# Kernel tuning notes

Measured on AMD Instinct MI355X. Metric: run time of the kernel, lower is better.

## Reference

```python
import jax, jax.numpy as jnp
import numpy as np

N = 100000      # nodes
E = 1600000     # edges (avg degree 16)
F_IN = 512      # nfeat
C = 64          # nclass


def setup_inputs() -> dict:
    key = jax.random.key(0)
    k1, k2, k3 = jax.random.split(key, 3)
    x = jax.random.normal(k1, (N, F_IN), dtype=jnp.float32)
    edge_index = jax.random.randint(k2, (2, E), 0, N, dtype=jnp.int32)
    # GCNConv weight (glorot-ish) and bias
    W = jax.random.normal(k3, (F_IN, C), dtype=jnp.float32) * (1.0 / np.sqrt(F_IN))
    b = jnp.zeros((C,), dtype=jnp.float32)
    return {"x": x, "W": W, "b": b, "edge_index": edge_index}


def reference(x, W, b, edge_index):
    # Standard GCNConv (sheaf_laplacian=None): project, add self-loops,
    # symmetric normalization D^{-1/2}(A+I)D^{-1/2}, aggregate, bias.
    h = x @ W  # [N, C] project first (C < F_IN), as torch_geometric does
    self_loops = jnp.arange(N, dtype=edge_index.dtype)
    src = jnp.concatenate([edge_index[0], self_loops])
    dst = jnp.concatenate([edge_index[1], self_loops])
    deg = jax.ops.segment_sum(jnp.ones_like(dst, dtype=h.dtype), dst, num_segments=N)
    dinv = jnp.where(deg > 0, jax.lax.rsqrt(deg), 0.0)  # deg^{-1/2}
    norm = dinv[src] * dinv[dst]  # [E+N]
    msgs = h[src] * norm[:, None]  # gather + scale, [E+N, C]
    out = jax.ops.segment_sum(msgs, dst, num_segments=N) + b  # [N, C]
    return jax.nn.log_softmax(out, axis=1)
```

## Files before the change

kernel.cpp:

```cpp
#include <hip/hip_runtime.h>
#include <hip/hip_bf16.h>

#define F_IN 512
#define NCLS 64
#define SCAN_BLK 512

typedef __attribute__((ext_vector_type(8))) short short8;
typedef __attribute__((ext_vector_type(4))) float f32x4;

static __device__ __forceinline__ short bf16_of(float f) {
    __hip_bfloat16 h = __float2bfloat16(f);
    short s;
    __builtin_memcpy(&s, &h, 2);
    return s;
}
static __device__ __forceinline__ float b2f(short s) {
    unsigned u = ((unsigned)(unsigned short)s) << 16;
    float f;
    __builtin_memcpy(&f, &u, 4);
    return f;
}

__global__ __launch_bounds__(256) void prelude(const float* __restrict__ W,
                                               short* __restrict__ Wb,
                                               int* __restrict__ cnt, int n) {
    const int bid = blockIdx.x;
    if (bid < 16) {
        int t = bid * 256 + threadIdx.x;
        int c = t >> 10;
        int kk = (t >> 6) & 15;
        int l = t & 63;
        short8 v;
#pragma unroll
        for (int j = 0; j < 8; ++j) {
            v[j] = bf16_of(W[(size_t)(kk * 32 + (l >> 4) * 8 + j) * NCLS + c * 16 + (l & 15)]);
        }
        reinterpret_cast<short8*>(Wb)[t] = v;
    } else {
        int i = (bid - 16) * 256 + threadIdx.x;
        if (i < n) cnt[i] = 0;
    }
}

__global__ __launch_bounds__(256) void megaA(const float* __restrict__ x,
                                             const short* __restrict__ Wb,
                                             short* __restrict__ g, int n,
                                             const int* __restrict__ dst,
                                             int* __restrict__ cnt,
                                             unsigned short* __restrict__ rank, int e,
                                             int gemmBlocks, int degBlocks) {
    const int bid = blockIdx.x;
    const int m2 = 2 * (gemmBlocks < degBlocks ? gemmBlocks : degBlocks);
    int role, idx;
    if (bid < m2) { role = bid & 1; idx = bid >> 1; }
    else if (gemmBlocks > degBlocks) { role = 0; idx = bid - degBlocks; }
    else { role = 1; idx = bid - gemmBlocks; }

    if (role == 1) {
        int base = (idx * 256 + threadIdx.x) * 4;
        if (base + 4 <= e) {
            int4 d4 = *reinterpret_cast<const int4*>(dst + base);
            ushort4 r;
            r.x = (unsigned short)atomicAdd(&cnt[d4.x], 1);
            r.y = (unsigned short)atomicAdd(&cnt[d4.y], 1);
            r.z = (unsigned short)atomicAdd(&cnt[d4.z], 1);
            r.w = (unsigned short)atomicAdd(&cnt[d4.w], 1);
            *reinterpret_cast<ushort4*>(rank + base) = r;
        } else {
            for (int i = base; i < e; ++i)
                rank[i] = (unsigned short)atomicAdd(&cnt[dst[i]], 1);
        }
        return;
    }

    const int wave = threadIdx.x >> 6;
    const int lane = threadIdx.x & 63;
    const int rowTile = idx * 64 + wave * 16;

    int arow = rowTile + (lane & 15);
    if (arow > n - 1) arow = n - 1;
    const float* xr = x + (size_t)arow * F_IN + ((lane >> 4) * 8);

    const short8* wb8 = reinterpret_cast<const short8*>(Wb);

    f32x4 acc0 = {0.f, 0.f, 0.f, 0.f};
    f32x4 acc1 = {0.f, 0.f, 0.f, 0.f};
    f32x4 acc2 = {0.f, 0.f, 0.f, 0.f};
    f32x4 acc3 = {0.f, 0.f, 0.f, 0.f};

#pragma unroll 4
    for (int kk = 0; kk < 16; ++kk) {
        float4 f0 = *reinterpret_cast<const float4*>(xr + kk * 32);
        float4 f1 = *reinterpret_cast<const float4*>(xr + kk * 32 + 4);
        short8 a;
        a[0] = bf16_of(f0.x); a[1] = bf16_of(f0.y);
        a[2] = bf16_of(f0.z); a[3] = bf16_of(f0.w);
        a[4] = bf16_of(f1.x); a[5] = bf16_of(f1.y);
        a[6] = bf16_of(f1.z); a[7] = bf16_of(f1.w);
        short8 b0 = wb8[(0 * 16 + kk) * 64 + lane];
        short8 b1 = wb8[(1 * 16 + kk) * 64 + lane];
        short8 b2 = wb8[(2 * 16 + kk) * 64 + lane];
        short8 b3 = wb8[(3 * 16 + kk) * 64 + lane];
        acc0 = __builtin_amdgcn_mfma_f32_16x16x32_bf16(a, b0, acc0, 0, 0, 0);
        acc1 = __builtin_amdgcn_mfma_f32_16x16x32_bf16(a, b1, acc1, 0, 0, 0);
        acc2 = __builtin_amdgcn_mfma_f32_16x16x32_bf16(a, b2, acc2, 0, 0, 0);
        acc3 = __builtin_amdgcn_mfma_f32_16x16x32_bf16(a, b3, acc3, 0, 0, 0);
    }

    const int col = lane & 15;
    const int rbase = rowTile + (lane >> 4) * 4;
#pragma unroll
    for (int j = 0; j < 4; ++j) {
        int r = rbase + j;
        if (r < n) {
            short* go = g + (size_t)r * NCLS + col;
            go[0]  = bf16_of(acc0[j]);
            go[16] = bf16_of(acc1[j]);
            go[32] = bf16_of(acc2[j]);
            go[48] = bf16_of(acc3[j]);
        }
    }
}

__global__ __launch_bounds__(SCAN_BLK) void scan1(const int* __restrict__ cnt,
                                                  int* __restrict__ off,
                                                  int* __restrict__ partials,
                                                  float* __restrict__ dinv, int n) {
    __shared__ int s[SCAN_BLK];
    int tid = threadIdx.x;
    int i = blockIdx.x * SCAN_BLK + tid;
    int v = (i < n) ? cnt[i] : 0;
    if (i < n) dinv[i] = rsqrtf(1.0f + (float)v);
    s[tid] = v;
    __syncthreads();
#pragma unroll
    for (int d = 1; d < SCAN_BLK; d <<= 1) {
        int t = (tid >= d) ? s[tid - d] : 0;
        __syncthreads();
        s[tid] += t;
        __syncthreads();
    }
    if (i < n) off[i] = s[tid] - v;
    if (i == n - 1) off[n] = s[tid];
    if (tid == SCAN_BLK - 1) partials[blockIdx.x] = s[tid];
}

__global__ __launch_bounds__(256) void scan2(int* __restrict__ partials, int p) {
    __shared__ int s[256];
    int tid = threadIdx.x;
    int v = (tid < p) ? partials[tid] : 0;
    s[tid] = v;
    __syncthreads();
#pragma unroll
    for (int d = 1; d < 256; d <<= 1) {
        int t = (tid >= d) ? s[tid - d] : 0;
        __syncthreads();
        s[tid] += t;
        __syncthreads();
    }
    if (tid < p) partials[tid] = s[tid] - v;
}

__global__ __launch_bounds__(256) void fill_csr(const int* __restrict__ src,
                                                const int* __restrict__ dst,
                                                const int* __restrict__ off,
                                                const int* __restrict__ parts,
                                                const unsigned short* __restrict__ rank,
                                                int* __restrict__ eidx, int e) {
    int base = (blockIdx.x * 256 + threadIdx.x) * 4;
    if (base + 4 <= e) {
        int4 s4 = *reinterpret_cast<const int4*>(src + base);
        int4 d4 = *reinterpret_cast<const int4*>(dst + base);
        ushort4 r4 = *reinterpret_cast<const ushort4*>(rank + base);
        eidx[off[d4.x] + parts[d4.x >> 9] + r4.x] = s4.x;
        eidx[off[d4.y] + parts[d4.y >> 9] + r4.y] = s4.y;
        eidx[off[d4.z] + parts[d4.z >> 9] + r4.z] = s4.z;
        eidx[off[d4.w] + parts[d4.w >> 9] + r4.w] = s4.w;
    } else {
        for (int i = base; i < e; ++i)
            eidx[off[dst[i]] + parts[dst[i] >> 9] + rank[i]] = src[i];
    }
}

__global__ __launch_bounds__(256) void aggregate(const short* __restrict__ g,
                                                 const float* __restrict__ dinv,
                                                 const float* __restrict__ b,
                                                 const int* __restrict__ off,
                                                 const int* __restrict__ parts,
                                                 const int* __restrict__ eidx,
                                                 float* __restrict__ out, int n) {
    const int wave = threadIdx.x >> 6;
    const int lane = threadIdx.x & 63;
    const int grp = lane >> 3;
    const int li = lane & 7;
    const int node = (blockIdx.x * 4 + wave) * 8 + grp;
    if (node >= n) return;

    const int s0 = off[node] + parts[node >> 9];
    const int np1 = node + 1;
    const int s1 = off[np1] + parts[(np1 == n ? n - 1 : np1) >> 9];

    const short8* g8 = reinterpret_cast<const short8*>(g);
    const float dn = dinv[node];

    float acc[8];
    {
        short8 v = g8[(size_t)node * 8 + li];
#pragma unroll
        for (int c = 0; c < 8; ++c) acc[c] = b2f(v[c]) * dn;
    }

    int t = s0;
    for (; t + 4 <= s1; t += 4) {
        int sa = eidx[t];
        int sb = eidx[t + 1];
        int sc = eidx[t + 2];
        int sd = eidx[t + 3];
        float da = dinv[sa], db = dinv[sb], dc = dinv[sc], dd = dinv[sd];
        short8 va = g8[(size_t)sa * 8 + li];
        short8 vb = g8[(size_t)sb * 8 + li];
        short8 vc = g8[(size_t)sc * 8 + li];
        short8 vd = g8[(size_t)sd * 8 + li];
#pragma unroll
        for (int c = 0; c < 8; ++c)
            acc[c] += (b2f(va[c]) * da + b2f(vb[c]) * db) + (b2f(vc[c]) * dc + b2f(vd[c]) * dd);
    }
    for (; t < s1; ++t) {
        int sa = eidx[t];
        float da = dinv[sa];
        short8 va = g8[(size_t)sa * 8 + li];
#pragma unroll
        for (int c = 0; c < 8; ++c) acc[c] += b2f(va[c]) * da;
    }

    const float4 b0 = reinterpret_cast<const float4*>(b)[li * 2];
    const float4 b1 = reinterpret_cast<const float4*>(b)[li * 2 + 1];
    float v[8];
    v[0] = acc[0] * dn + b0.x; v[1] = acc[1] * dn + b0.y;
    v[2] = acc[2] * dn + b0.z; v[3] = acc[3] * dn + b0.w;
    v[4] = acc[4] * dn + b1.x; v[5] = acc[5] * dn + b1.y;
    v[6] = acc[6] * dn + b1.z; v[7] = acc[7] * dn + b1.w;

    float m = v[0];
#pragma unroll
    for (int c = 1; c < 8; ++c) m = fmaxf(m, v[c]);
#pragma unroll
    for (int o = 1; o < 8; o <<= 1) m = fmaxf(m, __shfl_xor(m, o));

    float ex = 0.f;
#pragma unroll
    for (int c = 0; c < 8; ++c) ex += __expf(v[c] - m);
#pragma unroll
    for (int o = 1; o < 8; o <<= 1) ex += __shfl_xor(ex, o);
    const float lg = m + __logf(ex);

    float4 r0, r1;
    r0.x = v[0] - lg; r0.y = v[1] - lg; r0.z = v[2] - lg; r0.w = v[3] - lg;
    r1.x = v[4] - lg; r1.y = v[5] - lg; r1.z = v[6] - lg; r1.w = v[7] - lg;
    float4* o4 = reinterpret_cast<float4*>(out + (size_t)node * NCLS);
    o4[li * 2] = r0;
    o4[li * 2 + 1] = r1;
}

extern "C" void kernel_launch(void* const* d_in, const int* in_sizes, int n_in,
                              void* d_out, int out_size, void* d_ws, size_t ws_size,
                              hipStream_t stream) {
    const float* x = (const float*)d_in[0];
    const float* W = (const float*)d_in[1];
    const float* b = (const float*)d_in[2];
    const int* edge_index = (const int*)d_in[3];

    const int N = in_sizes[0] / F_IN;
    const int E = in_sizes[3] / 2;
    const int* src = edge_index;
    const int* dst = edge_index + E;

    float* out = (float*)d_out;

    char* ws = (char*)d_ws;
    short* g     = (short*)ws;  ws += (size_t)N * NCLS * 2;
    short* Wb    = (short*)ws;  ws += 4096 * 16;
    float* dinv  = (float*)ws;  ws += (size_t)N * 4;
    int*   cnt   = (int*)ws;    ws += (size_t)N * 4;
    int*   off   = (int*)ws;    ws += (size_t)(N + 4) * 4;
    int*   parts = (int*)ws;    ws += 1024 * 4;
    unsigned short* rank = (unsigned short*)ws;  ws += (size_t)((E + 7) & ~7) * 2;
    int*   eidx  = (int*)ws;

    const int nScanBlocks = (N + SCAN_BLK - 1) / SCAN_BLK;
    const int gemmBlocks = (N + 63) / 64;
    const int degBlocks = (E + 1023) / 1024;

    prelude<<<16 + (N + 255) / 256, 256, 0, stream>>>(W, Wb, cnt, N);

    megaA<<<gemmBlocks + degBlocks, 256, 0, stream>>>(x, Wb, g, N, dst, cnt, rank, E,
                                                      gemmBlocks, degBlocks);

    scan1<<<nScanBlocks, SCAN_BLK, 0, stream>>>(cnt, off, parts, dinv, N);
    scan2<<<1, 256, 0, stream>>>(parts, nScanBlocks);

    fill_csr<<<degBlocks, 256, 0, stream>>>(src, dst, off, parts, rank, eidx, E);

    aggregate<<<(N + 31) / 32, 256, 0, stream>>>(g, dinv, b, off, parts, eidx, out, N);
}
```

Baseline: 186.5 us.

## Fold source-degree scaling into GEMM epilogue and split degree count from GEMM

The megaA kernel, which interleaved GEMM blocks with degree-counting blocks, is split in two. The GEMM now runs after the degree scan, so each projected row can be pre-scaled by dinv[src] before it is stored in bf16. This removes the per-edge dinv gather from aggregation, whose inner loop is also widened to 8 edges for more memory-level parallelism. The GEMM tile grows to 32 rows per wave to reuse W loads. The cost is losing the overlap between the GEMM and the atomic degree counting, since they are now serialized.

```diff
diff --git a/kernel.cpp b/kernel.cpp
--- a/kernel.cpp
+++ b/kernel.cpp
@@ -42,83 +42,21 @@
     }
 }
 
-__global__ __launch_bounds__(256) void megaA(const float* __restrict__ x,
-                                             const short* __restrict__ Wb,
-                                             short* __restrict__ g, int n,
-                                             const int* __restrict__ dst,
-                                             int* __restrict__ cnt,
-                                             unsigned short* __restrict__ rank, int e,
-                                             int gemmBlocks, int degBlocks) {
-    const int bid = blockIdx.x;
-    const int m2 = 2 * (gemmBlocks < degBlocks ? gemmBlocks : degBlocks);
-    int role, idx;
-    if (bid < m2) { role = bid & 1; idx = bid >> 1; }
-    else if (gemmBlocks > degBlocks) { role = 0; idx = bid - degBlocks; }
-    else { role = 1; idx = bid - gemmBlocks; }
-
-    if (role == 1) {
-        int base = (idx * 256 + threadIdx.x) * 4;
-        if (base + 4 <= e) {
-            int4 d4 = *reinterpret_cast<const int4*>(dst + base);
-            ushort4 r;
-            r.x = (unsigned short)atomicAdd(&cnt[d4.x], 1);
-            r.y = (unsigned short)atomicAdd(&cnt[d4.y], 1);
-            r.z = (unsigned short)atomicAdd(&cnt[d4.z], 1);
-            r.w = (unsigned short)atomicAdd(&cnt[d4.w], 1);
-            *reinterpret_cast<ushort4*>(rank + base) = r;
-        } else {
-            for (int i = base; i < e; ++i)
-                rank[i] = (unsigned short)atomicAdd(&cnt[dst[i]], 1);
-        }
-        return;
-    }
-
-    const int wave = threadIdx.x >> 6;
-    const int lane = threadIdx.x & 63;
-    const int rowTile = idx * 64 + wave * 16;
-
-    int arow = rowTile + (lane & 15);
-    if (arow > n - 1) arow = n - 1;
-    const float* xr = x + (size_t)arow * F_IN + ((lane >> 4) * 8);
-
-    const short8* wb8 = reinterpret_cast<const short8*>(Wb);
-
-    f32x4 acc0 = {0.f, 0.f, 0.f, 0.f};
-    f32x4 acc1 = {0.f, 0.f, 0.f, 0.f};
-    f32x4 acc2 = {0.f, 0.f, 0.f, 0.f};
-    f32x4 acc3 = {0.f, 0.f, 0.f, 0.f};
-
-#pragma unroll 4
-    for (int kk = 0; kk < 16; ++kk) {
-        float4 f0 = *reinterpret_cast<const float4*>(xr + kk * 32);
-        float4 f1 = *reinterpret_cast<const float4*>(xr + kk * 32 + 4);
-        short8 a;
-        a[0] = bf16_of(f0.x); a[1] = bf16_of(f0.y);
-        a[2] = bf16_of(f0.z); a[3] = bf16_of(f0.w);
-        a[4] = bf16_of(f1.x); a[5] = bf16_of(f1.y);
-        a[6] = bf16_of(f1.z); a[7] = bf16_of(f1.w);
-        short8 b0 = wb8[(0 * 16 + kk) * 64 + lane];
-        short8 b1 = wb8[(1 * 16 + kk) * 64 + lane];
-        short8 b2 = wb8[(2 * 16 + kk) * 64 + lane];
-        short8 b3 = wb8[(3 * 16 + kk) * 64 + lane];
-        acc0 = __builtin_amdgcn_mfma_f32_16x16x32_bf16(a, b0, acc0, 0, 0, 0);
-        acc1 = __builtin_amdgcn_mfma_f32_16x16x32_bf16(a, b1, acc1, 0, 0, 0);
-        acc2 = __builtin_amdgcn_mfma_f32_16x16x32_bf16(a, b2, acc2, 0, 0, 0);
-        acc3 = __builtin_amdgcn_mfma_f32_16x16x32_bf16(a, b3, acc3, 0, 0, 0);
-    }
-
-    const int col = lane & 15;
-    const int rbase = rowTile + (lane >> 4) * 4;
-#pragma unroll
-    for (int j = 0; j < 4; ++j) {
-        int r = rbase + j;
-        if (r < n) {
-            short* go = g + (size_t)r * NCLS + col;
-            go[0]  = bf16_of(acc0[j]);
-            go[16] = bf16_of(acc1[j]);
-            go[32] = bf16_of(acc2[j]);
-            go[48] = bf16_of(acc3[j]);
-        }
+__global__ __launch_bounds__(256) void deg_count(const int* __restrict__ dst,
+                                                 int* __restrict__ cnt,
+                                                 unsigned short* __restrict__ rank, int e) {
+    int base = (blockIdx.x * 256 + threadIdx.x) * 4;
+    if (base + 4 <= e) {
+        int4 d4 = *reinterpret_cast<const int4*>(dst + base);
+        ushort4 r;
+        r.x = (unsigned short)atomicAdd(&cnt[d4.x], 1);
+        r.y = (unsigned short)atomicAdd(&cnt[d4.y], 1);
+        r.z = (unsigned short)atomicAdd(&cnt[d4.z], 1);
+        r.w = (unsigned short)atomicAdd(&cnt[d4.w], 1);
+        *reinterpret_cast<ushort4*>(rank + base) = r;
+    } else {
+        for (int i = base; i < e; ++i)
+            rank[i] = (unsigned short)atomicAdd(&cnt[dst[i]], 1);
     }
 }
 
@@ -182,6 +120,77 @@
     }
 }
 
+__global__ __launch_bounds__(256) void gemm_mfma(const float* __restrict__ x,
+                                                 const short* __restrict__ Wb,
+                                                 const float* __restrict__ dinv,
+                                                 short* __restrict__ g, int n) {
+    const int wave = threadIdx.x >> 6;
+    const int lane = threadIdx.x & 63;
+    const int rowTile = blockIdx.x * 128 + wave * 32;
+
+    int r0 = rowTile + (lane & 15);
+    int r1 = r0 + 16;
+    if (r0 > n - 1) r0 = n - 1;
+    if (r1 > n - 1) r1 = n - 1;
+    const float* xr0 = x + (size_t)r0 * F_IN + ((lane >> 4) * 8);
+    const float* xr1 = x + (size_t)r1 * F_IN + ((lane >> 4) * 8);
+
+    const short8* wb8 = reinterpret_cast<const short8*>(Wb);
+
+    f32x4 acc[2][4];
+#pragma unroll
+    for (int h = 0; h < 2; ++h)
+#pragma unroll
+        for (int c = 0; c < 4; ++c) acc[h][c] = {0.f, 0.f, 0.f, 0.f};
+
+#pragma unroll 4
+    for (int kk = 0; kk < 16; ++kk) {
+        float4 p0 = *reinterpret_cast<const float4*>(xr0 + kk * 32);
+        float4 p1 = *reinterpret_cast<const float4*>(xr0 + kk * 32 + 4);
+        float4 q0 = *reinterpret_cast<const float4*>(xr1 + kk * 32);
+        float4 q1 = *reinterpret_cast<const float4*>(xr1 + kk * 32 + 4);
+        short8 a0, a1;
+        a0[0] = bf16_of(p0.x); a0[1] = bf16_of(p0.y);
+        a0[2] = bf16_of(p0.z); a0[3] = bf16_of(p0.w);
+        a0[4] = bf16_of(p1.x); a0[5] = bf16_of(p1.y);
+        a0[6] = bf16_of(p1.z); a0[7] = bf16_of(p1.w);
+        a1[0] = bf16_of(q0.x); a1[1] = bf16_of(q0.y);
+        a1[2] = bf16_of(q0.z); a1[3] = bf16_of(q0.w);
+        a1[4] = bf16_of(q1.x); a1[5] = bf16_of(q1.y);
+        a1[6] = bf16_of(q1.z); a1[7] = bf16_of(q1.w);
+        short8 b0 = wb8[(0 * 16 + kk) * 64 + lane];
+        short8 b1 = wb8[(1 * 16 + kk) * 64 + lane];
+        short8 b2 = wb8[(2 * 16 + kk) * 64 + lane];
+        short8 b3 = wb8[(3 * 16 + kk) * 64 + lane];
+        acc[0][0] = __builtin_amdgcn_mfma_f32_16x16x32_bf16(a0, b0, acc[0][0], 0, 0, 0);
+        acc[0][1] = __builtin_amdgcn_mfma_f32_16x16x32_bf16(a0, b1, acc[0][1], 0, 0, 0);
+        acc[0][2] = __builtin_amdgcn_mfma_f32_16x16x32_bf16(a0, b2, acc[0][2], 0, 0, 0);
+        acc[0][3] = __builtin_amdgcn_mfma_f32_16x16x32_bf16(a0, b3, acc[0][3], 0, 0, 0);
+        acc[1][0] = __builtin_amdgcn_mfma_f32_16x16x32_bf16(a1, b0, acc[1][0], 0, 0, 0);
+        acc[1][1] = __builtin_amdgcn_mfma_f32_16x16x32_bf16(a1, b1, acc[1][1], 0, 0, 0);
+        acc[1][2] = __builtin_amdgcn_mfma_f32_16x16x32_bf16(a1, b2, acc[1][2], 0, 0, 0);
+        acc[1][3] = __builtin_amdgcn_mfma_f32_16x16x32_bf16(a1, b3, acc[1][3], 0, 0, 0);
+    }
+
+    const int col = lane & 15;
+#pragma unroll
+    for (int h = 0; h < 2; ++h) {
+        const int rbase = rowTile + h * 16 + (lane >> 4) * 4;
+#pragma unroll
+        for (int j = 0; j < 4; ++j) {
+            int r = rbase + j;
+            if (r < n) {
+                float dv = dinv[r];
+                short* go = g + (size_t)r * NCLS + col;
+                go[0]  = bf16_of(acc[h][0][j] * dv);
+                go[16] = bf16_of(acc[h][1][j] * dv);
+                go[32] = bf16_of(acc[h][2][j] * dv);
+                go[48] = bf16_of(acc[h][3][j] * dv);
+            }
+        }
+    }
+}
+
 __global__ __launch_bounds__(256) void aggregate(const short* __restrict__ g,
                                                  const float* __restrict__ dinv,
                                                  const float* __restrict__ b,
@@ -201,38 +210,45 @@
     const int s1 = off[np1] + parts[(np1 == n ? n - 1 : np1) >> 9];
 
     const short8* g8 = reinterpret_cast<const short8*>(g);
-    const float dn = dinv[node];
 
     float acc[8];
     {
         short8 v = g8[(size_t)node * 8 + li];
 #pragma unroll
-        for (int c = 0; c < 8; ++c) acc[c] = b2f(v[c]) * dn;
+        for (int c = 0; c < 8; ++c) acc[c] = b2f(v[c]);
     }
 
     int t = s0;
+    for (; t + 8 <= s1; t += 8) {
+        int sidx[8];
+#pragma unroll
+        for (int u = 0; u < 8; ++u) sidx[u] = eidx[t + u];
+        short8 vv[8];
+#pragma unroll
+        for (int u = 0; u < 8; ++u) vv[u] = g8[(size_t)sidx[u] * 8 + li];
+#pragma unroll
+        for (int c = 0; c < 8; ++c)
+            acc[c] += ((b2f(vv[0][c]) + b2f(vv[1][c])) + (b2f(vv[2][c]) + b2f(vv[3][c]))) +
+                      ((b2f(vv[4][c]) + b2f(vv[5][c])) + (b2f(vv[6][c]) + b2f(vv[7][c])));
+    }
     for (; t + 4 <= s1; t += 4) {
-        int sa = eidx[t];
-        int sb = eidx[t + 1];
-        int sc = eidx[t + 2];
-        int sd = eidx[t + 3];
-        float da = dinv[sa], db = dinv[sb], dc = dinv[sc], dd = dinv[sd];
+        int sa = eidx[t], sb = eidx[t + 1], sc = eidx[t + 2], sd = eidx[t + 3];
         short8 va = g8[(size_t)sa * 8 + li];
         short8 vb = g8[(size_t)sb * 8 + li];
         short8 vc = g8[(size_t)sc * 8 + li];
         short8 vd = g8[(size_t)sd * 8 + li];
 #pragma unroll
         for (int c = 0; c < 8; ++c)
-            acc[c] += (b2f(va[c]) * da + b2f(vb[c]) * db) + (b2f(vc[c]) * dc + b2f(vd[c]) * dd);
+            acc[c] += (b2f(va[c]) + b2f(vb[c])) + (b2f(vc[c]) + b2f(vd[c]));
     }
     for (; t < s1; ++t) {
         int sa = eidx[t];
-        float da = dinv[sa];
         short8 va = g8[(size_t)sa * 8 + li];
 #pragma unroll
-        for (int c = 0; c < 8; ++c) acc[c] += b2f(va[c]) * da;
-    }
-
+        for (int c = 0; c < 8; ++c) acc[c] += b2f(va[c]);
+    }
+
+    const float dn = dinv[node];
     const float4 b0 = reinterpret_cast<const float4*>(b)[li * 2];
     const float4 b1 = reinterpret_cast<const float4*>(b)[li * 2 + 1];
     float v[8];
@@ -288,18 +304,18 @@
     int*   eidx  = (int*)ws;
 
     const int nScanBlocks = (N + SCAN_BLK - 1) / SCAN_BLK;
-    const int gemmBlocks = (N + 63) / 64;
-    const int degBlocks = (E + 1023) / 1024;
+    const int edgeBlocks = (E + 1023) / 1024;
 
     prelude<<<16 + (N + 255) / 256, 256, 0, stream>>>(W, Wb, cnt, N);
 
-    megaA<<<gemmBlocks + degBlocks, 256, 0, stream>>>(x, Wb, g, N, dst, cnt, rank, E,
-                                                      gemmBlocks, degBlocks);
+    deg_count<<<edgeBlocks, 256, 0, stream>>>(dst, cnt, rank, E);
 
     scan1<<<nScanBlocks, SCAN_BLK, 0, stream>>>(cnt, off, parts, dinv, N);
     scan2<<<1, 256, 0, stream>>>(parts, nScanBlocks);
 
-    fill_csr<<<degBlocks, 256, 0, stream>>>(src, dst, off, parts, rank, eidx, E);
+    gemm_mfma<<<(N + 127) / 128, 256, 0, stream>>>(x, Wb, dinv, g, N);
+
+    fill_csr<<<edgeBlocks, 256, 0, stream>>>(src, dst, off, parts, rank, eidx, E);
 
     aggregate<<<(N + 31) / 32, 256, 0, stream>>>(g, dinv, b, off, parts, eidx, out, N);
 }
```

After: 191.0 us. 1.02x slower.
